# Optimization experiments

Measured on AMD Instinct MI355X. Metric: run time of the kernel, lower is better.

Reference implementation:

```python
import jax, jax.numpy as jnp
import numpy as np

NUM_SINK = 8   # cfg.SINKHORN_ITERS
MASS = 0.9     # marginal value used for a and b


def _graph_conv(x, W_enc, b_enc, W1, b1, W2, b2, k):
    # Node encoder
    h = jax.nn.relu(x @ W_enc + b_enc)                       # [G,M,D]
    # kNN in embedding space (per graph)
    sq = jnp.sum(h * h, axis=-1)                             # [G,M]
    d2 = sq[:, :, None] + sq[:, None, :] - 2.0 * jnp.einsum('gmd,gnd->gmn', h, h)
    d2 = d2 + jnp.eye(h.shape[1], dtype=h.dtype) * 1e9       # exclude self-loop
    _, idx = jax.lax.top_k(-d2, k)                           # [G,M,k]
    neigh = jax.vmap(lambda hg, ig: hg[ig])(h, idx)          # [G,M,k,D]
    hc = jnp.broadcast_to(h[:, :, None, :], neigh.shape)
    e = jnp.concatenate([hc, neigh - hc], axis=-1)           # [G,M,k,2D]
    e = jax.nn.relu(e @ W1 + b1)                             # edge embed
    e = e @ W2 + b2                                          # back to D
    return jnp.max(e, axis=2)                                # max-aggregate over neighbors


def _sinkhorn(cost, lam):
    # log-domain unrolled Sinkhorn, batched over graphs; a=b=0.9 marginals
    log_p = -cost / lam                                      # [G,M,N]
    log_m = jnp.log(jnp.asarray(MASS, cost.dtype))
    for _ in range(NUM_SINK - 1):
        log_p = log_p - (jax.nn.logsumexp(log_p, axis=2, keepdims=True) - log_m)
        log_p = log_p - (jax.nn.logsumexp(log_p, axis=1, keepdims=True) - log_m)
    log_p = log_p - (jax.nn.logsumexp(log_p, axis=2, keepdims=True) - log_m)
    return jnp.exp(log_p)


def setup_inputs() -> dict:
    key = jax.random.key(0)
    ks = jax.random.split(key, 6)
    G, M, D = 64, 256, 256
    E = 256  # edge embed size
    inp = {
        'tra_x': jax.random.normal(ks[0], (G, M, D), jnp.float32),
        'det_x': jax.random.normal(ks[1], (G, M, D), jnp.float32),
        'W_enc': jax.random.normal(ks[2], (D, D), jnp.float32) / np.sqrt(D),
        'b_enc': jnp.zeros((D,), jnp.float32),
        'W1': jax.random.normal(ks[3], (2 * D, E), jnp.float32) / np.sqrt(2 * D),
        'b1': jnp.zeros((E,), jnp.float32),
        'W2': jax.random.normal(ks[4], (E, D), jnp.float32) / np.sqrt(E),
        'b2': jnp.zeros((D,), jnp.float32),
        'eplison': jnp.zeros((1,), jnp.float32),
        'k': 16,
    }
    return inp


def reference(tra_x, det_x, W_enc, b_enc, W1, b1, W2, b2, eplison, k):
    tra = _graph_conv(tra_x, W_enc, b_enc, W1, b1, W2, b2, k)  # [G,M,D]
    det = _graph_conv(det_x, W_enc, b_enc, W1, b1, W2, b2, k)  # [G,N,D]
    corr = jnp.einsum('gmd,gnd->gmn', tra, det)
    n1 = jnp.linalg.norm(tra, axis=-1)                         # [G,M]
    n2 = jnp.linalg.norm(det, axis=-1)                         # [G,N]
    cost = -corr / (n1[:, :, None] * n2[:, None, :])
    lam = jnp.exp(eplison[0]) + 0.03
    return _sinkhorn(cost, lam)                                # [G,M,N]
```

## Files before the change

kernel.cpp:

```cpp
#include <hip/hip_runtime.h>
#include <math.h>

#define NG 64
#define NM 256
#define ND 256
#define NK 16
#define NR (NG * NM)
#define NB 32

#define MASSF 0.9f

typedef __attribute__((ext_vector_type(8))) short bf16x8;
typedef __attribute__((ext_vector_type(4))) float f32x4;

static __device__ __forceinline__ short f2bf(float x) {
  union {
    float f;
    unsigned u;
  } v;
  v.f = x;
  unsigned r = v.u + 0x7FFFu + ((v.u >> 16) & 1u);
  return (short)(r >> 16);
}
static __device__ __forceinline__ float bf2f(short x) {
  union {
    unsigned u;
    float f;
  } v;
  v.u = ((unsigned)(unsigned short)x) << 16;
  return v.f;
}

__global__ __launch_bounds__(256) void prep_k(const float* __restrict__ W1,
                                              const float* __restrict__ b1,
                                              const float* __restrict__ W2,
                                              short* __restrict__ w2t, short* __restrict__ w1cat,
                                              float* __restrict__ biascat) {
  const int b = blockIdx.x, k = threadIdx.x;
  if (b < 256) {
    w2t[b * 256 + k] = f2bf(W2[(size_t)k * 256 + b]);
  } else {
    const int n = b - 256;
    float v;
    if (n < 256)
      v = W1[(size_t)k * 256 + n] - W1[(size_t)(k + 256) * 256 + n];
    else
      v = W1[(size_t)(k + 256) * 256 + (n - 256)];
    w1cat[(size_t)n * 256 + k] = f2bf(v);
    if (k == 0) biascat[n] = (n < 256) ? b1[n] : 0.f;
  }
}

template <bool RELU, bool BIAS, bool WBF>
__global__ __launch_bounds__(256) void gemm_nn_k(const float* __restrict__ A,
                                                 const float* __restrict__ B,
                                                 const float* __restrict__ bias,
                                                 float* __restrict__ C, short* __restrict__ Cbf,
                                                 int N, int K) {
  __shared__ float As[16][68];
  __shared__ float Bs[16][64];
  const int tid = threadIdx.x;
  const int tx = tid & 15, ty = tid >> 4;
  const int m0 = blockIdx.y * 64, n0 = blockIdx.x * 64;
  float acc[4][4] = {};
  const int ar = tid >> 2, akc = (tid & 3) * 4;
  const int bkr = tid >> 4, bc = (tid & 15) * 4;
  for (int k0 = 0; k0 < K; k0 += 16) {
    float4 av = *(const float4*)&A[(size_t)(m0 + ar) * K + k0 + akc];
    As[akc + 0][ar] = av.x;
    As[akc + 1][ar] = av.y;
    As[akc + 2][ar] = av.z;
    As[akc + 3][ar] = av.w;
    *(float4*)&Bs[bkr][bc] = *(const float4*)&B[(size_t)(k0 + bkr) * N + n0 + bc];
    __syncthreads();
#pragma unroll
    for (int kk = 0; kk < 16; ++kk) {
      const float4 a = *(const float4*)&As[kk][ty * 4];
      const float4 b = *(const float4*)&Bs[kk][tx * 4];
      const float aa[4] = {a.x, a.y, a.z, a.w};
      const float bb[4] = {b.x, b.y, b.z, b.w};
#pragma unroll
      for (int i = 0; i < 4; ++i)
#pragma unroll
        for (int j = 0; j < 4; ++j) acc[i][j] = fmaf(aa[i], bb[j], acc[i][j]);
    }
    __syncthreads();
  }
  float4 bv = {0.f, 0.f, 0.f, 0.f};
  if (BIAS) bv = *(const float4*)&bias[n0 + tx * 4];
#pragma unroll
  for (int i = 0; i < 4; ++i) {
    float4 o = {acc[i][0], acc[i][1], acc[i][2], acc[i][3]};
    if (BIAS) {
      o.x += bv.x;
      o.y += bv.y;
      o.z += bv.z;
      o.w += bv.w;
    }
    if (RELU) {
      o.x = fmaxf(o.x, 0.f);
      o.y = fmaxf(o.y, 0.f);
      o.z = fmaxf(o.z, 0.f);
      o.w = fmaxf(o.w, 0.f);
    }
    const size_t off = (size_t)(m0 + ty * 4 + i) * N + n0 + tx * 4;
    *(float4*)&C[off] = o;
    if (WBF) {
      short4 hb = {f2bf(o.x), f2bf(o.y), f2bf(o.z), f2bf(o.w)};
      *(short4*)&Cbf[off] = hb;
    }
  }
}

__global__ __launch_bounds__(256) void gemm_nt_k(const float* __restrict__ A,
                                                 const float* __restrict__ B,
                                                 float* __restrict__ C) {
  __shared__ float As[16][68];
  __shared__ float Bs[16][68];
  const int g = blockIdx.z;
  const float* Ag = A + (size_t)g * NM * ND;
  const float* Bg = B + (size_t)g * NM * ND;
  const int tid = threadIdx.x;
  const int tx = tid & 15, ty = tid >> 4;
  const int m0 = blockIdx.y * 64, n0 = blockIdx.x * 64;
  float acc[4][4] = {};
  const int r = tid >> 2, kc = (tid & 3) * 4;
  for (int k0 = 0; k0 < ND; k0 += 16) {
    float4 av = *(const float4*)&Ag[(size_t)(m0 + r) * ND + k0 + kc];
    As[kc + 0][r] = av.x;
    As[kc + 1][r] = av.y;
    As[kc + 2][r] = av.z;
    As[kc + 3][r] = av.w;
    float4 bvv = *(const float4*)&Bg[(size_t)(n0 + r) * ND + k0 + kc];
    Bs[kc + 0][r] = bvv.x;
    Bs[kc + 1][r] = bvv.y;
    Bs[kc + 2][r] = bvv.z;
    Bs[kc + 3][r] = bvv.w;
    __syncthreads();
#pragma unroll
    for (int kk = 0; kk < 16; ++kk) {
      const float4 a = *(const float4*)&As[kk][ty * 4];
      const float4 b = *(const float4*)&Bs[kk][tx * 4];
      const float aa[4] = {a.x, a.y, a.z, a.w};
      const float bb[4] = {b.x, b.y, b.z, b.w};
#pragma unroll
      for (int i = 0; i < 4; ++i)
#pragma unroll
        for (int j = 0; j < 4; ++j) acc[i][j] = fmaf(aa[i], bb[j], acc[i][j]);
    }
    __syncthreads();
  }
#pragma unroll
  for (int i = 0; i < 4; ++i) {
    const int m = m0 + ty * 4 + i;
    float4 o = {acc[i][0], acc[i][1], acc[i][2], acc[i][3]};
    *(float4*)&C[(size_t)g * NM * NM + (size_t)m * NM + n0 + tx * 4] = o;
  }
}

__global__ __launch_bounds__(256, 2) void mlp1_mfma_k(const short* __restrict__ A,
                                                      const short* __restrict__ Bt,
                                                      const float* __restrict__ biascat,
                                                      short* __restrict__ baseb,
                                                      short* __restrict__ n1b) {
  __shared__ char As[64 * 512];
  const int tid = threadIdx.x;
  const int l = tid & 63, wv = tid >> 6;
  const int r = l & 15, gq = l >> 4;
  const int m0 = blockIdx.y * 64, n0 = blockIdx.x * 128;
  bf16x8 bfr[2][8];
  float bv[2];
#pragma unroll
  for (int nt = 0; nt < 2; ++nt) {
    const int col = n0 + wv * 32 + nt * 16 + r;
    const short* wb = Bt + (size_t)col * 256 + gq * 8;
#pragma unroll
    for (int ks = 0; ks < 8; ++ks) bfr[nt][ks] = *(const bf16x8*)(wb + ks * 32);
    bv[nt] = biascat[col];
  }
  const int row = tid >> 2, ch = tid & 3;
  const char* ag = (const char*)(A + (size_t)(m0 + row) * 256) + ch * 128;
  char* lb = As + row * 512;
#pragma unroll
  for (int j = 0; j < 8; ++j)
    *(bf16x8*)(lb + (((ch * 128 + j * 16)) ^ ((row & 7) << 4))) = *(const bf16x8*)(ag + j * 16);
  __syncthreads();
  f32x4 acc[4][2];
#pragma unroll
  for (int mt = 0; mt < 4; ++mt)
#pragma unroll
    for (int nt = 0; nt < 2; ++nt) acc[mt][nt] = (f32x4){0.f, 0.f, 0.f, 0.f};
#pragma unroll
  for (int ks = 0; ks < 8; ++ks) {
    bf16x8 a[4];
#pragma unroll
    for (int mt = 0; mt < 4; ++mt)
      a[mt] = *(const bf16x8*)(As + (mt * 16 + r) * 512 + ((gq * 16 + ks * 64) ^ ((r & 7) << 4)));
#pragma unroll
    for (int mt = 0; mt < 4; ++mt)
#pragma unroll
      for (int nt = 0; nt < 2; ++nt)
        acc[mt][nt] = __builtin_amdgcn_mfma_f32_16x16x32_bf16(a[mt], bfr[nt][ks], acc[mt][nt], 0, 0, 0);
  }
  short* dst = (n0 < 256) ? baseb : n1b;
  const int cb = (n0 < 256) ? n0 : n0 - 256;
#pragma unroll
  for (int mt = 0; mt < 4; ++mt)
#pragma unroll
    for (int nt = 0; nt < 2; ++nt) {
      const int col = cb + wv * 32 + nt * 16 + r;
#pragma unroll
      for (int reg = 0; reg < 4; ++reg) {
        const int rw = m0 + mt * 16 + gq * 4 + reg;
        dst[(size_t)rw * 256 + col] = f2bf(acc[mt][nt][reg] + bv[nt]);
      }
    }
}

__global__ __launch_bounds__(256, 2) void cost_mfma_k(const short* __restrict__ featT,
                                                      const short* __restrict__ featD,
                                                      const float* __restrict__ nA,
                                                      const float* __restrict__ nB,
                                                      const float* __restrict__ eps,
                                                      float* __restrict__ P) {
  __shared__ char As[64 * 512];
  const int g = blockIdx.z;
  const short* A = featT + (size_t)g * NM * ND;
  const short* Bt = featD + (size_t)g * NM * ND;
  const int tid = threadIdx.x;
  const int l = tid & 63, wv = tid >> 6;
  const int r = l & 15, gq = l >> 4;
  const int m0 = blockIdx.y * 64, n0 = blockIdx.x * 128;
  bf16x8 bfr[2][8];
  float rnb[2];
#pragma unroll
  for (int nt = 0; nt < 2; ++nt) {
    const int col = n0 + wv * 32 + nt * 16 + r;
    const short* wb = Bt + (size_t)col * 256 + gq * 8;
#pragma unroll
    for (int ks = 0; ks < 8; ++ks) bfr[nt][ks] = *(const bf16x8*)(wb + ks * 32);
    rnb[nt] = 1.0f / nB[g * NM + col];
  }
  const int row = tid >> 2, ch = tid & 3;
  const char* ag = (const char*)(A + (size_t)(m0 + row) * 256) + ch * 128;
  char* lb = As + row * 512;
#pragma unroll
  for (int j = 0; j < 8; ++j)
    *(bf16x8*)(lb + (((ch * 128 + j * 16)) ^ ((row & 7) << 4))) = *(const bf16x8*)(ag + j * 16);
  __syncthreads();
  f32x4 acc[4][2];
#pragma unroll
  for (int mt = 0; mt < 4; ++mt)
#pragma unroll
    for (int nt = 0; nt < 2; ++nt) acc[mt][nt] = (f32x4){0.f, 0.f, 0.f, 0.f};
#pragma unroll
  for (int ks = 0; ks < 8; ++ks) {
    bf16x8 a[4];
#pragma unroll
    for (int mt = 0; mt < 4; ++mt)
      a[mt] = *(const bf16x8*)(As + (mt * 16 + r) * 512 + ((gq * 16 + ks * 64) ^ ((r & 7) << 4)));
#pragma unroll
    for (int mt = 0; mt < 4; ++mt)
#pragma unroll
      for (int nt = 0; nt < 2; ++nt)
        acc[mt][nt] = __builtin_amdgcn_mfma_f32_16x16x32_bf16(a[mt], bfr[nt][ks], acc[mt][nt], 0, 0, 0);
  }
  const float inv_lam = 1.0f / (expf(eps[0]) + 0.03f);
#pragma unroll
  for (int mt = 0; mt < 4; ++mt) {
    float ria[4];
#pragma unroll
    for (int reg = 0; reg < 4; ++reg)
      ria[reg] = inv_lam / nA[g * NM + m0 + mt * 16 + gq * 4 + reg];
#pragma unroll
    for (int nt = 0; nt < 2; ++nt) {
      const int col = n0 + wv * 32 + nt * 16 + r;
#pragma unroll
      for (int reg = 0; reg < 4; ++reg) {
        const int rw = m0 + mt * 16 + gq * 4 + reg;
        P[(size_t)g * NM * NM + (size_t)rw * 256 + col] =
            expf(acc[mt][nt][reg] * ria[reg] * rnb[nt]);
      }
    }
  }
}

__global__ __launch_bounds__(256) void rowsq_k(const float* __restrict__ h,
                                               float* __restrict__ sq) {
  const int w = threadIdx.x >> 6, lane = threadIdx.x & 63;
  const int row = blockIdx.x * 4 + w;
  float4 v = *(const float4*)&h[(size_t)row * ND + lane * 4];
  float s = v.x * v.x + v.y * v.y + v.z * v.z + v.w * v.w;
#pragma unroll
  for (int off = 32; off; off >>= 1) s += __shfl_xor(s, off);
  if (lane == 0) sq[row] = s;
}

__global__ __launch_bounds__(256) void normrow_bf_k(const short* __restrict__ feat,
                                                    float* __restrict__ nrm) {
  const int w = threadIdx.x >> 6, lane = threadIdx.x & 63;
  const int row = blockIdx.x * 4 + w;
  const short4 v = *(const short4*)&feat[(size_t)row * ND + lane * 4];
  const float a = bf2f(v.x), b = bf2f(v.y), c = bf2f(v.z), d = bf2f(v.w);
  float s = a * a + b * b + c * c + d * d;
#pragma unroll
  for (int off = 32; off; off >>= 1) s += __shfl_xor(s, off);
  if (lane == 0) nrm[row] = sqrtf(s);
}

__global__ __launch_bounds__(256) void topk_k(const float* __restrict__ S,
                                              const float* __restrict__ sq,
                                              int* __restrict__ idx) {
  const int w = threadIdx.x >> 6, lane = threadIdx.x & 63;
  const int row = blockIdx.x * 4 + w;
  const int g = row >> 8, m = row & 255;
  const float* Srow = S + (size_t)row * NM;
  const float* sqg = sq + g * NM;
  const float sm = sqg[m];
  const float4 sv = *(const float4*)&Srow[lane * 4];
  const float4 qv = *(const float4*)&sqg[lane * 4];
  float cand[4] = {sm + qv.x - 2.f * sv.x, sm + qv.y - 2.f * sv.y, sm + qv.z - 2.f * sv.z,
                   sm + qv.w - 2.f * sv.w};
#pragma unroll
  for (int t = 0; t < 4; ++t)
    if (lane * 4 + t == m) cand[t] = 1e30f;
  for (int rnd = 0; rnd < NK; ++rnd) {
    float bvv = cand[0];
    int bi = lane * 4;
#pragma unroll
    for (int t = 1; t < 4; ++t)
      if (cand[t] < bvv) {
        bvv = cand[t];
        bi = lane * 4 + t;
      }
#pragma unroll
    for (int off = 1; off < 64; off <<= 1) {
      const float ov = __shfl_xor(bvv, off);
      const int oi = __shfl_xor(bi, off);
      if (ov < bvv || (ov == bvv && oi < bi)) {
        bvv = ov;
        bi = oi;
      }
    }
    if (lane == 0) idx[(size_t)row * NK + rnd] = bi;
    if ((bi >> 2) == lane) cand[bi & 3] = 1e30f;
  }
}

__global__ __launch_bounds__(512, 4) void edgemlp_mfma3_k(
    const short* __restrict__ baseb, const short* __restrict__ n1b, const int* __restrict__ idx,
    const short* __restrict__ w2t, const float* __restrict__ b2, short* __restrict__ featbf) {
  __shared__ short E[2][16 * 256];
  __shared__ int sidx[NB * NK];
  const int tid = threadIdx.x;
  const int l = tid & 63, wv = tid >> 6;
  const int node0 = blockIdx.x * NB;
  const int g = node0 >> 8;
  const int r = l & 15, gq = l >> 4;
  sidx[tid] = idx[(size_t)node0 * NK + tid];
  bf16x8 bfr[2][8];
  float b2v[2];
#pragma unroll
  for (int t = 0; t < 2; ++t) {
    const int nb = wv * 2 + t;
    const short* wb = w2t + (size_t)(nb * 16 + r) * 256 + gq * 8;
#pragma unroll
    for (int ks = 0; ks < 8; ++ks) bfr[t][ks] = *(const bf16x8*)(wb + ks * 32);
    b2v[t] = b2[nb * 16 + r];
  }
  __syncthreads();
  const int srow = tid >> 5, sc = (tid & 31) * 8;
  const int wbyte = ((srow * 512 + sc * 2) ^ ((srow & 7) << 4));
  bf16x8 bs, ns;
  auto sload = [&](int i) {
    bs = *(const bf16x8*)(baseb + (((size_t)(node0 + i)) << 8) + sc);
    ns = *(const bf16x8*)(n1b + ((((size_t)g << 8) + sidx[i * NK + srow]) << 8) + sc);
  };
  sload(0);
  for (int i = 0; i < NB; ++i) {
    const int buf = i & 1;
    bf16x8 w0;
#pragma unroll
    for (int j = 0; j < 8; ++j) w0[j] = f2bf(fmaxf(bf2f(bs[j]) + bf2f(ns[j]), 0.f));
    *(bf16x8*)((char*)&E[buf][0] + wbyte) = w0;
    __syncthreads();
    if (i + 1 < NB) sload(i + 1);
    f32x4 acc[2];
    acc[0] = (f32x4){0.f, 0.f, 0.f, 0.f};
    acc[1] = (f32x4){0.f, 0.f, 0.f, 0.f};
    const char* eb = (const char*)&E[buf][0];
    const int abase = r * 512 + gq * 16;
#pragma unroll
    for (int ks = 0; ks < 8; ++ks) {
      const bf16x8 a = *(const bf16x8*)(eb + ((abase + ks * 64) ^ ((r & 7) << 4)));
      acc[0] = __builtin_amdgcn_mfma_f32_16x16x32_bf16(a, bfr[0][ks], acc[0], 0, 0, 0);
      acc[1] = __builtin_amdgcn_mfma_f32_16x16x32_bf16(a, bfr[1][ks], acc[1], 0, 0, 0);
    }
#pragma unroll
    for (int t = 0; t < 2; ++t) {
      float m1 = fmaxf(fmaxf(acc[t][0], acc[t][1]), fmaxf(acc[t][2], acc[t][3]));
      m1 = fmaxf(m1, __shfl_xor(m1, 16));
      m1 = fmaxf(m1, __shfl_xor(m1, 32));
      if (gq == 0)
        featbf[(((size_t)(node0 + i)) << 8) + (wv * 2 + t) * 16 + r] = f2bf(m1 + b2v[t]);
    }
  }
}

__global__ __launch_bounds__(1024) void sinkhorn_k(float* __restrict__ P) {
  __shared__ float red[16][256];
  __shared__ float scal[256];
  const int t = threadIdx.x;
  const int tc = t & 15;
  const int trw = t >> 4;
  const int wv = t >> 6, l = t & 63;
  float* Pg = P + (size_t)blockIdx.x * NM * NM;
  float p[4][16];
#pragma unroll
  for (int i = 0; i < 4; ++i)
#pragma unroll
    for (int q = 0; q < 4; ++q)
      *(f32x4*)&p[i][q * 4] = *(const f32x4*)&Pg[(size_t)(trw * 4 + i) * NM + tc * 16 + q * 4];

  auto rowpass = [&]() {
#pragma unroll
    for (int i = 0; i < 4; ++i) {
      float s = p[i][0];
#pragma unroll
      for (int j = 1; j < 16; ++j) s += p[i][j];
      s += __shfl_xor(s, 1);
      s += __shfl_xor(s, 2);
      s += __shfl_xor(s, 4);
      s += __shfl_xor(s, 8);
      const float sc = MASSF / s;
#pragma unroll
      for (int j = 0; j < 16; ++j) p[i][j] *= sc;
    }
  };
  auto colpass = [&]() {
    float tmp[16];
#pragma unroll
    for (int j = 0; j < 16; ++j) tmp[j] = ((p[0][j] + p[1][j]) + (p[2][j] + p[3][j]));
#pragma unroll
    for (int j = 0; j < 16; ++j) {
      tmp[j] += __shfl_xor(tmp[j], 16);
      tmp[j] += __shfl_xor(tmp[j], 32);
    }
    if (l < 16) {
#pragma unroll
      for (int q = 0; q < 4; ++q)
        *(f32x4*)&red[wv][l * 16 + q * 4] = *(const f32x4*)&tmp[q * 4];
    }
    __syncthreads();
    if (t < 256) {
      float s = red[0][t];
#pragma unroll
      for (int w = 1; w < 16; ++w) s += red[w][t];
      scal[t] = MASSF / s;
    }
    __syncthreads();
#pragma unroll
    for (int j = 0; j < 16; ++j) {
      const float sc = scal[tc * 16 + j];
#pragma unroll
      for (int i = 0; i < 4; ++i) p[i][j] *= sc;
    }
    __syncthreads();
  };
  for (int it = 0; it < 7; ++it) {
    rowpass();
    colpass();
  }
  rowpass();
#pragma unroll
  for (int i = 0; i < 4; ++i)
#pragma unroll
    for (int q = 0; q < 4; ++q)
      *(f32x4*)&Pg[(size_t)(trw * 4 + i) * NM + tc * 16 + q * 4] = *(const f32x4*)&p[i][q * 4];
}

extern "C" void kernel_launch(void* const* d_in, const int* in_sizes, int n_in, void* d_out,
                              int out_size, void* d_ws, size_t ws_size, hipStream_t stream) {
  const float* tra_x = (const float*)d_in[0];
  const float* det_x = (const float*)d_in[1];
  const float* W_enc = (const float*)d_in[2];
  const float* b_enc = (const float*)d_in[3];
  const float* W1 = (const float*)d_in[4];
  const float* b1 = (const float*)d_in[5];
  const float* W2 = (const float*)d_in[6];
  const float* b2 = (const float*)d_in[7];
  const float* eps = (const float*)d_in[8];
  float* out = (float*)d_out;

  const size_t SZ = (size_t)NR * ND;
  float* h = (float*)d_ws;
  short* hbf = (short*)(h + SZ);
  short* baseb = hbf + SZ;
  short* n1b = baseb + SZ;
  short* featT = n1b + SZ;
  short* featD = featT + SZ;
  float* sq = (float*)(featD + SZ);
  float* nT = sq + NR;
  float* nD = nT + NR;
  int* idx = (int*)(nD + NR);
  short* w2t = (short*)(idx + (size_t)NR * NK);
  short* w1cat = w2t + 256 * 256;
  float* biascat = (float*)(w1cat + 512 * 256);
  float* S = out;

  const float* xs[2] = {tra_x, det_x};
  short* feats[2] = {featT, featD};
  float* nrms[2] = {nT, nD};

  prep_k<<<768, 256, 0, stream>>>(W1, b1, W2, w2t, w1cat, biascat);
  for (int s2 = 0; s2 < 2; ++s2) {
    gemm_nn_k<true, true, true>
        <<<dim3(4, 256), 256, 0, stream>>>(xs[s2], W_enc, b_enc, h, hbf, 256, 256);
    mlp1_mfma_k<<<dim3(4, 256), 256, 0, stream>>>(hbf, w1cat, biascat, baseb, n1b);
    rowsq_k<<<4096, 256, 0, stream>>>(h, sq);
    gemm_nt_k<<<dim3(4, 4, NG), 256, 0, stream>>>(h, h, S);
    topk_k<<<4096, 256, 0, stream>>>(S, sq, idx);
    edgemlp_mfma3_k<<<NR / NB, 512, 0, stream>>>(baseb, n1b, idx, w2t, b2, feats[s2]);
    normrow_bf_k<<<4096, 256, 0, stream>>>(feats[s2], nrms[s2]);
  }
  cost_mfma_k<<<dim3(2, 4, NG), 256, 0, stream>>>(featT, featD, nT, nD, eps, out);
  sinkhorn_k<<<NG, 1024, 0, stream>>>(out);
}
```

Baseline: 401.3 us.

## Widen FP32 GEMM tiles with double buffering, exploit Gram symmetry, batch edge MLP

The encoder GEMM and per-graph Gram GEMM now use 64x128 tiles with register-prefetched, double-buffered shared memory, so there is one barrier per k-step and more FMAs per shared load. The Gram kernel skips the lower-left blocks and writes their values as the transpose of the mirrored blocks, cutting that matmul work by roughly a quarter. The edge MLP kernel stages two nodes per iteration, which halves its barrier count and overlaps neighbour gathers with the MFMA work. In exchange, register and LDS use per block grow, and the transposed stores to S are strided.

```diff
diff --git a/kernel.cpp b/kernel.cpp
--- a/kernel.cpp
+++ b/kernel.cpp
@@ -51,110 +51,145 @@
   }
 }
 
-template <bool RELU, bool BIAS, bool WBF>
-__global__ __launch_bounds__(256) void gemm_nn_k(const float* __restrict__ A,
-                                                 const float* __restrict__ B,
-                                                 const float* __restrict__ bias,
-                                                 float* __restrict__ C, short* __restrict__ Cbf,
-                                                 int N, int K) {
-  __shared__ float As[16][68];
-  __shared__ float Bs[16][64];
+__global__ __launch_bounds__(256) void gemm_nn2_k(const float* __restrict__ A,
+                                                  const float* __restrict__ B,
+                                                  const float* __restrict__ bias,
+                                                  float* __restrict__ C,
+                                                  short* __restrict__ Cbf) {
+  __shared__ float As[2][16][68];
+  __shared__ float Bs[2][16][128];
   const int tid = threadIdx.x;
   const int tx = tid & 15, ty = tid >> 4;
-  const int m0 = blockIdx.y * 64, n0 = blockIdx.x * 64;
-  float acc[4][4] = {};
-  const int ar = tid >> 2, akc = (tid & 3) * 4;
-  const int bkr = tid >> 4, bc = (tid & 15) * 4;
-  for (int k0 = 0; k0 < K; k0 += 16) {
-    float4 av = *(const float4*)&A[(size_t)(m0 + ar) * K + k0 + akc];
-    As[akc + 0][ar] = av.x;
-    As[akc + 1][ar] = av.y;
-    As[akc + 2][ar] = av.z;
-    As[akc + 3][ar] = av.w;
-    *(float4*)&Bs[bkr][bc] = *(const float4*)&B[(size_t)(k0 + bkr) * N + n0 + bc];
+  const int m0 = blockIdx.y * 64, n0 = blockIdx.x * 128;
+  const int arow = tid >> 2, akc = (tid & 3) * 4;
+  const int bkr = tid >> 4, bcc = (tid & 15) * 4;
+  float4 av, bv0, bv1;
+  float acc[4][8] = {};
+  auto gload = [&](int k0) {
+    av = *(const float4*)&A[(size_t)(m0 + arow) * 256 + k0 + akc];
+    bv0 = *(const float4*)&B[(size_t)(k0 + bkr) * 256 + n0 + bcc];
+    bv1 = *(const float4*)&B[(size_t)(k0 + bkr) * 256 + n0 + 64 + bcc];
+  };
+  auto swrite = [&](int buf) {
+    As[buf][akc + 0][arow] = av.x;
+    As[buf][akc + 1][arow] = av.y;
+    As[buf][akc + 2][arow] = av.z;
+    As[buf][akc + 3][arow] = av.w;
+    *(float4*)&Bs[buf][bkr][bcc] = bv0;
+    *(float4*)&Bs[buf][bkr][64 + bcc] = bv1;
+  };
+  gload(0);
+  swrite(0);
+  __syncthreads();
+  for (int s = 0; s < 16; ++s) {
+    if (s < 15) gload((s + 1) * 16);
+    const int buf = s & 1;
+#pragma unroll
+    for (int kk = 0; kk < 16; ++kk) {
+      const float4 a0 = *(const float4*)&As[buf][kk][ty * 4];
+      const float4 b0 = *(const float4*)&Bs[buf][kk][tx * 4];
+      const float4 b1 = *(const float4*)&Bs[buf][kk][64 + tx * 4];
+      const float aa[4] = {a0.x, a0.y, a0.z, a0.w};
+      const float bb[8] = {b0.x, b0.y, b0.z, b0.w, b1.x, b1.y, b1.z, b1.w};
+#pragma unroll
+      for (int i = 0; i < 4; ++i)
+#pragma unroll
+        for (int j = 0; j < 8; ++j) acc[i][j] = fmaf(aa[i], bb[j], acc[i][j]);
+    }
+    if (s < 15) swrite((s + 1) & 1);
     __syncthreads();
-#pragma unroll
-    for (int kk = 0; kk < 16; ++kk) {
-      const float4 a = *(const float4*)&As[kk][ty * 4];
-      const float4 b = *(const float4*)&Bs[kk][tx * 4];
-      const float aa[4] = {a.x, a.y, a.z, a.w};
-      const float bb[4] = {b.x, b.y, b.z, b.w};
-#pragma unroll
-      for (int i = 0; i < 4; ++i)
-#pragma unroll
-        for (int j = 0; j < 4; ++j) acc[i][j] = fmaf(aa[i], bb[j], acc[i][j]);
-    }
-    __syncthreads();
-  }
-  float4 bv = {0.f, 0.f, 0.f, 0.f};
-  if (BIAS) bv = *(const float4*)&bias[n0 + tx * 4];
+  }
+  const float4 bia0 = *(const float4*)&bias[n0 + tx * 4];
+  const float4 bia1 = *(const float4*)&bias[n0 + 64 + tx * 4];
 #pragma unroll
   for (int i = 0; i < 4; ++i) {
-    float4 o = {acc[i][0], acc[i][1], acc[i][2], acc[i][3]};
-    if (BIAS) {
-      o.x += bv.x;
-      o.y += bv.y;
-      o.z += bv.z;
-      o.w += bv.w;
-    }
-    if (RELU) {
-      o.x = fmaxf(o.x, 0.f);
-      o.y = fmaxf(o.y, 0.f);
-      o.z = fmaxf(o.z, 0.f);
-      o.w = fmaxf(o.w, 0.f);
-    }
-    const size_t off = (size_t)(m0 + ty * 4 + i) * N + n0 + tx * 4;
-    *(float4*)&C[off] = o;
-    if (WBF) {
-      short4 hb = {f2bf(o.x), f2bf(o.y), f2bf(o.z), f2bf(o.w)};
-      *(short4*)&Cbf[off] = hb;
-    }
-  }
-}
-
-__global__ __launch_bounds__(256) void gemm_nt_k(const float* __restrict__ A,
-                                                 const float* __restrict__ B,
-                                                 float* __restrict__ C) {
-  __shared__ float As[16][68];
-  __shared__ float Bs[16][68];
-  const int g = blockIdx.z;
-  const float* Ag = A + (size_t)g * NM * ND;
-  const float* Bg = B + (size_t)g * NM * ND;
+    const size_t row = (size_t)(m0 + ty * 4 + i);
+    float4 o0 = {fmaxf(acc[i][0] + bia0.x, 0.f), fmaxf(acc[i][1] + bia0.y, 0.f),
+                 fmaxf(acc[i][2] + bia0.z, 0.f), fmaxf(acc[i][3] + bia0.w, 0.f)};
+    float4 o1 = {fmaxf(acc[i][4] + bia1.x, 0.f), fmaxf(acc[i][5] + bia1.y, 0.f),
+                 fmaxf(acc[i][6] + bia1.z, 0.f), fmaxf(acc[i][7] + bia1.w, 0.f)};
+    *(float4*)&C[row * 256 + n0 + tx * 4] = o0;
+    *(float4*)&C[row * 256 + n0 + 64 + tx * 4] = o1;
+    short4 h0 = {f2bf(o0.x), f2bf(o0.y), f2bf(o0.z), f2bf(o0.w)};
+    short4 h1 = {f2bf(o1.x), f2bf(o1.y), f2bf(o1.z), f2bf(o1.w)};
+    *(short4*)&Cbf[row * 256 + n0 + tx * 4] = h0;
+    *(short4*)&Cbf[row * 256 + n0 + 64 + tx * 4] = h1;
+  }
+}
+
+__global__ __launch_bounds__(256) void gemm_nt2_k(const float* __restrict__ h,
+                                                  float* __restrict__ C) {
+  const int bx = blockIdx.x, by = blockIdx.y, g = blockIdx.z;
+  if (bx == 0 && by >= 2) return;
+  __shared__ float As[2][16][68];
+  __shared__ float Bs[2][16][128];
+  const float* Ag = h + (size_t)g * NM * ND;
+  float* Cg = C + (size_t)g * NM * NM;
   const int tid = threadIdx.x;
   const int tx = tid & 15, ty = tid >> 4;
-  const int m0 = blockIdx.y * 64, n0 = blockIdx.x * 64;
-  float acc[4][4] = {};
-  const int r = tid >> 2, kc = (tid & 3) * 4;
-  for (int k0 = 0; k0 < ND; k0 += 16) {
-    float4 av = *(const float4*)&Ag[(size_t)(m0 + r) * ND + k0 + kc];
-    As[kc + 0][r] = av.x;
-    As[kc + 1][r] = av.y;
-    As[kc + 2][r] = av.z;
-    As[kc + 3][r] = av.w;
-    float4 bvv = *(const float4*)&Bg[(size_t)(n0 + r) * ND + k0 + kc];
-    Bs[kc + 0][r] = bvv.x;
-    Bs[kc + 1][r] = bvv.y;
-    Bs[kc + 2][r] = bvv.z;
-    Bs[kc + 3][r] = bvv.w;
+  const int m0 = by * 64, n0 = bx * 128;
+  const int arow = tid >> 2, akc = (tid & 3) * 4;
+  const int brow = tid >> 1, bkc = (tid & 1) * 8;
+  float4 av, bva, bvb;
+  float acc[4][8] = {};
+  auto gload = [&](int k0) {
+    av = *(const float4*)&Ag[(size_t)(m0 + arow) * 256 + k0 + akc];
+    bva = *(const float4*)&Ag[(size_t)(n0 + brow) * 256 + k0 + bkc];
+    bvb = *(const float4*)&Ag[(size_t)(n0 + brow) * 256 + k0 + bkc + 4];
+  };
+  auto swrite = [&](int buf) {
+    As[buf][akc + 0][arow] = av.x;
+    As[buf][akc + 1][arow] = av.y;
+    As[buf][akc + 2][arow] = av.z;
+    As[buf][akc + 3][arow] = av.w;
+    Bs[buf][bkc + 0][brow] = bva.x;
+    Bs[buf][bkc + 1][brow] = bva.y;
+    Bs[buf][bkc + 2][brow] = bva.z;
+    Bs[buf][bkc + 3][brow] = bva.w;
+    Bs[buf][bkc + 4][brow] = bvb.x;
+    Bs[buf][bkc + 5][brow] = bvb.y;
+    Bs[buf][bkc + 6][brow] = bvb.z;
+    Bs[buf][bkc + 7][brow] = bvb.w;
+  };
+  gload(0);
+  swrite(0);
+  __syncthreads();
+  for (int s = 0; s < 16; ++s) {
+    if (s < 15) gload((s + 1) * 16);
+    const int buf = s & 1;
+#pragma unroll
+    for (int kk = 0; kk < 16; ++kk) {
+      const float4 a0 = *(const float4*)&As[buf][kk][ty * 4];
+      const float4 b0 = *(const float4*)&Bs[buf][kk][tx * 4];
+      const float4 b1 = *(const float4*)&Bs[buf][kk][64 + tx * 4];
+      const float aa[4] = {a0.x, a0.y, a0.z, a0.w};
+      const float bb[8] = {b0.x, b0.y, b0.z, b0.w, b1.x, b1.y, b1.z, b1.w};
+#pragma unroll
+      for (int i = 0; i < 4; ++i)
+#pragma unroll
+        for (int j = 0; j < 8; ++j) acc[i][j] = fmaf(aa[i], bb[j], acc[i][j]);
+    }
+    if (s < 15) swrite((s + 1) & 1);
     __syncthreads();
-#pragma unroll
-    for (int kk = 0; kk < 16; ++kk) {
-      const float4 a = *(const float4*)&As[kk][ty * 4];
-      const float4 b = *(const float4*)&Bs[kk][tx * 4];
-      const float aa[4] = {a.x, a.y, a.z, a.w};
-      const float bb[4] = {b.x, b.y, b.z, b.w};
-#pragma unroll
-      for (int i = 0; i < 4; ++i)
-#pragma unroll
-        for (int j = 0; j < 4; ++j) acc[i][j] = fmaf(aa[i], bb[j], acc[i][j]);
-    }
-    __syncthreads();
   }
 #pragma unroll
   for (int i = 0; i < 4; ++i) {
-    const int m = m0 + ty * 4 + i;
-    float4 o = {acc[i][0], acc[i][1], acc[i][2], acc[i][3]};
-    *(float4*)&C[(size_t)g * NM * NM + (size_t)m * NM + n0 + tx * 4] = o;
+    const size_t row = (size_t)(m0 + ty * 4 + i);
+    float4 o0 = {acc[i][0], acc[i][1], acc[i][2], acc[i][3]};
+    float4 o1 = {acc[i][4], acc[i][5], acc[i][6], acc[i][7]};
+    *(float4*)&Cg[row * 256 + n0 + tx * 4] = o0;
+    *(float4*)&Cg[row * 256 + n0 + 64 + tx * 4] = o1;
+  }
+  if (bx == 1 && by < 2) {
+#pragma unroll
+    for (int j = 0; j < 4; ++j) {
+      const size_t col0 = (size_t)(n0 + tx * 4 + j);
+      const size_t col1 = (size_t)(n0 + 64 + tx * 4 + j);
+      float4 t0 = {acc[0][j], acc[1][j], acc[2][j], acc[3][j]};
+      float4 t1 = {acc[0][4 + j], acc[1][4 + j], acc[2][4 + j], acc[3][4 + j]};
+      *(float4*)&Cg[col0 * 256 + m0 + ty * 4] = t0;
+      *(float4*)&Cg[col1 * 256 + m0 + ty * 4] = t1;
+    }
   }
 }
 
@@ -347,10 +382,10 @@
   }
 }
 
-__global__ __launch_bounds__(512, 4) void edgemlp_mfma3_k(
+__global__ __launch_bounds__(512, 4) void edgemlp_mfma4_k(
     const short* __restrict__ baseb, const short* __restrict__ n1b, const int* __restrict__ idx,
     const short* __restrict__ w2t, const float* __restrict__ b2, short* __restrict__ featbf) {
-  __shared__ short E[2][16 * 256];
+  __shared__ short E[2][32 * 256];
   __shared__ int sidx[NB * NK];
   const int tid = threadIdx.x;
   const int l = tid & 63, wv = tid >> 6;
@@ -369,41 +404,60 @@
     b2v[t] = b2[nb * 16 + r];
   }
   __syncthreads();
-  const int srow = tid >> 5, sc = (tid & 31) * 8;
-  const int wbyte = ((srow * 512 + sc * 2) ^ ((srow & 7) << 4));
-  bf16x8 bs, ns;
-  auto sload = [&](int i) {
-    bs = *(const bf16x8*)(baseb + (((size_t)(node0 + i)) << 8) + sc);
-    ns = *(const bf16x8*)(n1b + ((((size_t)g << 8) + sidx[i * NK + srow]) << 8) + sc);
+  const int j = tid >> 5;
+  const int c = (tid & 31) * 8;
+  const unsigned wboff = (unsigned)((c * 2) ^ ((j & 7) << 4));
+  bf16x8 ns0, ns1;
+  auto sload = [&](int s) {
+    const int nb0 = s * 2;
+    ns0 = *(const bf16x8*)(n1b + ((((size_t)g << 8) + sidx[nb0 * NK + j]) << 8) + c);
+    ns1 = *(const bf16x8*)(n1b + ((((size_t)g << 8) + sidx[(nb0 + 1) * NK + j]) << 8) + c);
+  };
+  auto swrite = [&](int s) {
+    char* eb = (char*)&E[s & 1][0];
+    const int nb0 = s * 2;
+    const bf16x8 b0 = *(const bf16x8*)(baseb + (((size_t)(node0 + nb0)) << 8) + c);
+    const bf16x8 b1 = *(const bf16x8*)(baseb + (((size_t)(node0 + nb0 + 1)) << 8) + c);
+    bf16x8 w0, w1;
+#pragma unroll
+    for (int q = 0; q < 8; ++q) {
+      w0[q] = f2bf(fmaxf(bf2f(b0[q]) + bf2f(ns0[q]), 0.f));
+      w1[q] = f2bf(fmaxf(bf2f(b1[q]) + bf2f(ns1[q]), 0.f));
+    }
+    *(bf16x8*)(eb + (size_t)j * 512 + wboff) = w0;
+    *(bf16x8*)(eb + (size_t)(16 + j) * 512 + wboff) = w1;
   };
   sload(0);
-  for (int i = 0; i < NB; ++i) {
-    const int buf = i & 1;
-    bf16x8 w0;
-#pragma unroll
-    for (int j = 0; j < 8; ++j) w0[j] = f2bf(fmaxf(bf2f(bs[j]) + bf2f(ns[j]), 0.f));
-    *(bf16x8*)((char*)&E[buf][0] + wbyte) = w0;
+  swrite(0);
+  __syncthreads();
+  for (int s = 0; s < NB / 2; ++s) {
+    if (s + 1 < NB / 2) sload(s + 1);
+    const char* eb = (const char*)&E[s & 1][0];
+#pragma unroll
+    for (int q = 0; q < 2; ++q) {
+      f32x4 acc0 = (f32x4){0.f, 0.f, 0.f, 0.f};
+      f32x4 acc1 = (f32x4){0.f, 0.f, 0.f, 0.f};
+      const int rowb = (q * 16 + r) * 512;
+#pragma unroll
+      for (int ks = 0; ks < 8; ++ks) {
+        const bf16x8 a = *(const bf16x8*)(eb + rowb + ((gq * 16 + ks * 64) ^ ((r & 7) << 4)));
+        acc0 = __builtin_amdgcn_mfma_f32_16x16x32_bf16(a, bfr[0][ks], acc0, 0, 0, 0);
+        acc1 = __builtin_amdgcn_mfma_f32_16x16x32_bf16(a, bfr[1][ks], acc1, 0, 0, 0);
+      }
+      const int nd = node0 + s * 2 + q;
+      float m0v = fmaxf(fmaxf(acc0[0], acc0[1]), fmaxf(acc0[2], acc0[3]));
+      m0v = fmaxf(m0v, __shfl_xor(m0v, 16));
+      m0v = fmaxf(m0v, __shfl_xor(m0v, 32));
+      float m1v = fmaxf(fmaxf(acc1[0], acc1[1]), fmaxf(acc1[2], acc1[3]));
+      m1v = fmaxf(m1v, __shfl_xor(m1v, 16));
+      m1v = fmaxf(m1v, __shfl_xor(m1v, 32));
+      if (gq == 0) {
+        featbf[((size_t)nd << 8) + (wv * 2 + 0) * 16 + r] = f2bf(m0v + b2v[0]);
+        featbf[((size_t)nd << 8) + (wv * 2 + 1) * 16 + r] = f2bf(m1v + b2v[1]);
+      }
+    }
+    if (s + 1 < NB / 2) swrite(s + 1);
     __syncthreads();
-    if (i + 1 < NB) sload(i + 1);
-    f32x4 acc[2];
-    acc[0] = (f32x4){0.f, 0.f, 0.f, 0.f};
-    acc[1] = (f32x4){0.f, 0.f, 0.f, 0.f};
-    const char* eb = (const char*)&E[buf][0];
-    const int abase = r * 512 + gq * 16;
-#pragma unroll
-    for (int ks = 0; ks < 8; ++ks) {
-      const bf16x8 a = *(const bf16x8*)(eb + ((abase + ks * 64) ^ ((r & 7) << 4)));
-      acc[0] = __builtin_amdgcn_mfma_f32_16x16x32_bf16(a, bfr[0][ks], acc[0], 0, 0, 0);
-      acc[1] = __builtin_amdgcn_mfma_f32_16x16x32_bf16(a, bfr[1][ks], acc[1], 0, 0, 0);
-    }
-#pragma unroll
-    for (int t = 0; t < 2; ++t) {
-      float m1 = fmaxf(fmaxf(acc[t][0], acc[t][1]), fmaxf(acc[t][2], acc[t][3]));
-      m1 = fmaxf(m1, __shfl_xor(m1, 16));
-      m1 = fmaxf(m1, __shfl_xor(m1, 32));
-      if (gq == 0)
-        featbf[(((size_t)(node0 + i)) << 8) + (wv * 2 + t) * 16 + r] = f2bf(m1 + b2v[t]);
-    }
   }
 }
 
@@ -514,13 +568,12 @@
 
   prep_k<<<768, 256, 0, stream>>>(W1, b1, W2, w2t, w1cat, biascat);
   for (int s2 = 0; s2 < 2; ++s2) {
-    gemm_nn_k<true, true, true>
-        <<<dim3(4, 256), 256, 0, stream>>>(xs[s2], W_enc, b_enc, h, hbf, 256, 256);
+    gemm_nn2_k<<<dim3(2, 256), 256, 0, stream>>>(xs[s2], W_enc, b_enc, h, hbf);
     mlp1_mfma_k<<<dim3(4, 256), 256, 0, stream>>>(hbf, w1cat, biascat, baseb, n1b);
     rowsq_k<<<4096, 256, 0, stream>>>(h, sq);
-    gemm_nt_k<<<dim3(4, 4, NG), 256, 0, stream>>>(h, h, S);
+    gemm_nt2_k<<<dim3(2, 4, NG), 256, 0, stream>>>(h, S);
     topk_k<<<4096, 256, 0, stream>>>(S, sq, idx);
-    edgemlp_mfma3_k<<<NR / NB, 512, 0, stream>>>(baseb, n1b, idx, w2t, b2, feats[s2]);
+    edgemlp_mfma4_k<<<NR / NB, 512, 0, stream>>>(baseb, n1b, idx, w2t, b2, feats[s2]);
     normrow_bf_k<<<4096, 256, 0, stream>>>(feats[s2], nrms[s2]);
   }
   cost_mfma_k<<<dim3(2, 4, NG), 256, 0, stream>>>(featT, featD, nT, nD, eps, out);
```

Measured after the change: 398.7 us. Within noise of the previous version (-0.6%).
